# Performance work log

Measured on AMD Instinct MI355X. Metric: run time of the kernel, lower is better.

## Reference

```python
import jax, jax.numpy as jnp
import numpy as np

B, S, D, H = 4, 2048, 1024, 16
DK = D // H
THETA = 10000.0


def setup_inputs() -> dict:
    key = jax.random.key(0)
    ks = jax.random.split(key, 5)
    std = (2.0 / (D + D)) ** 0.5  # Linear init std (distribution differs from trunc-normal; math identical)
    x = jax.random.normal(ks[0], (B, S, D), dtype=jnp.float32)
    wq = jax.random.normal(ks[1], (D, D), dtype=jnp.float32) * std
    wk = jax.random.normal(ks[2], (D, D), dtype=jnp.float32) * std
    wv = jax.random.normal(ks[3], (D, D), dtype=jnp.float32) * std
    wo = jax.random.normal(ks[4], (D, D), dtype=jnp.float32) * std
    mask = jnp.tril(jnp.ones((S, S), dtype=bool))  # causal
    return {"x": x, "mask": mask, "wq": wq, "wk": wk, "wv": wv, "wo": wo}


def _rope(t):
    # t: [b, h, s, dk]; interleaved pairs (even, odd)
    s = t.shape[-2]
    inv_freq = THETA ** (-jnp.arange(0, DK, 2, dtype=jnp.float32) / DK)  # [dk/2]
    ang = jnp.arange(s, dtype=jnp.float32)[:, None] * inv_freq[None, :]  # [s, dk/2]
    cos = jnp.cos(ang)[None, None, :, :]
    sin = jnp.sin(ang)[None, None, :, :]
    x1 = t[..., 0::2]
    x2 = t[..., 1::2]
    rot = jnp.stack([x1 * cos - x2 * sin, x1 * sin + x2 * cos], axis=-1)
    return rot.reshape(t.shape)


def reference(x, mask, wq, wk, wv, wo):
    b, s, d = x.shape
    def heads(w):
        return jnp.einsum('bsd,ed->bse', x, w).reshape(b, s, H, DK).transpose(0, 2, 1, 3)
    q = _rope(heads(wq))
    k = _rope(heads(wk))
    v = heads(wv)
    scores = jnp.einsum('bhqd,bhkd->bhqk', q, k) / (DK ** 0.5)
    scores = jnp.where(mask, scores, -jnp.inf)
    attn = jax.nn.softmax(scores, axis=-1)
    out = jnp.einsum('bhqk,bhkd->bhqd', attn, v)
    out = out.transpose(0, 2, 1, 3).reshape(b, s, d)
    return jnp.einsum('bsd,ed->bse', out, wo)
```

## Files before the change

kernel.cpp:

```cpp
#include <hip/hip_runtime.h>

constexpr int Bc = 4, Sc = 2048, Dc = 1024, Hc = 16, DKc = 64;
constexpr int Mc = Bc * Sc;

typedef __bf16 bf16x8 __attribute__((ext_vector_type(8)));
typedef float f32x4 __attribute__((ext_vector_type(4)));
typedef unsigned short ush;

#define DEVI __device__ __forceinline__

DEVI ush bf(float f) { return __builtin_bit_cast(ush, (__bf16)f); }

DEVI void ld_lds16(const void* g, void* l) {
    __builtin_amdgcn_global_load_lds(
        (const __attribute__((address_space(1))) unsigned int*)g,
        (__attribute__((address_space(3))) unsigned int*)l,
        16, 0, 0);
}

constexpr unsigned CVT_BLOCKS = 6144;
constexpr unsigned TAB_BLOCKS = 32;

__global__ __launch_bounds__(256) void cvt_all(
    const float* __restrict__ x,  const float* __restrict__ wq,
    const float* __restrict__ wk, const float* __restrict__ wv,
    const float* __restrict__ wo, ush* __restrict__ dst,
    float2* __restrict__ csn)
{
    if (blockIdx.x >= CVT_BLOCKS) {
        int t = (int)(blockIdx.x - CVT_BLOCKS) * 256 + threadIdx.x;
#pragma unroll
        for (int i = 0; i < 8; i++) {
            int idx = t * 8 + i;
            int s = idx >> 5, p = idx & 31;
            float ang = (float)s * exp2f(-(float)p * 0.4152410118609203f);
            csn[idx] = make_float2(cosf(ang), sinf(ang));
        }
        return;
    }
    size_t t = ((size_t)blockIdx.x * 256 + threadIdx.x) * 8;
    const float* src; size_t loc;
    const size_t NX = (size_t)Mc * Dc;
    if (t < NX) { src = x; loc = t; }
    else {
        size_t u = t - NX;
        int wi = (int)(u >> 20);
        src = (wi == 0) ? wq : ((wi == 1) ? wk : ((wi == 2) ? wv : wo));
        loc = u & 1048575u;
    }
    float4 a = *(const float4*)(src + loc);
    float4 b = *(const float4*)(src + loc + 4);
    union { ush u[8]; float4 v; } o;
    o.u[0] = bf(a.x); o.u[1] = bf(a.y); o.u[2] = bf(a.z); o.u[3] = bf(a.w);
    o.u[4] = bf(b.x); o.u[5] = bf(b.y); o.u[6] = bf(b.z); o.u[7] = bf(b.w);
    *(float4*)(dst + t) = o.v;
}

template<int MODE>
__global__ __launch_bounds__(512, 4) void gemm_bf(
    const ush* __restrict__ A,
    const ush* __restrict__ W0, const ush* __restrict__ W1,
    const ush* __restrict__ W2,
    ush* __restrict__ Oq, ush* __restrict__ Ok, ush* __restrict__ Ovt,
    float* __restrict__ Of, const float2* __restrict__ csn)
{
    __shared__ ush sA[128 * 64];
    __shared__ ush sB[128 * 64];

    const int xcd = (int)blockIdx.x;
    const int u = (int)blockIdx.y + 64 * (int)blockIdx.z;
    const int z = (MODE == 0) ? (u >> 6) : 0;
    const int w = u & 63;
    const int m0 = (xcd * 8 + (w >> 3)) * 128;
    const int n0 = (w & 7) * 128;

    const ush* W = (z == 0) ? W0 : ((z == 1) ? W1 : W2);

    const int tid = threadIdx.x;
    const int wv = tid >> 6;
    const int ln = tid & 63;
    const int lr = ln & 15;
    const int lq = ln >> 4;
    const int wm = (wv & 1) * 64;
    const int wn = (wv >> 1) * 32;
    const int rL = ln >> 3;
    const int cSw = ((ln & 7) ^ rL) * 8;
    const int ca0 = lq ^ (ln & 7);

    f32x4 acc[4][2] = {};
    const bool swp = (MODE == 0) && (z == 2);

    for (int kt = 0; kt < 1024; kt += 64) {
        __syncthreads();
#pragma unroll
        for (int i = 0; i < 2; i++) {
            int chunk = wv * 2 + i;
            int rr = chunk * 8 + rL;
            ld_lds16(&A[(size_t)(m0 + rr) * 1024 + kt + cSw], &sA[chunk * 512]);
            ld_lds16(&W[(size_t)(n0 + rr) * 1024 + kt + cSw], &sB[chunk * 512]);
        }
        __syncthreads();
#pragma unroll
        for (int ks = 0; ks < 2; ks++) {
            const int cf = (ca0 ^ (ks << 2)) << 3;
            bf16x8 af[4], bfr[2];
#pragma unroll
            for (int t = 0; t < 4; t++)
                af[t]  = *(const bf16x8*)(&sA[(wm + t * 16 + lr) * 64 + cf]);
#pragma unroll
            for (int t = 0; t < 2; t++)
                bfr[t] = *(const bf16x8*)(&sB[(wn + t * 16 + lr) * 64 + cf]);
            __builtin_amdgcn_s_setprio(1);
            if (!swp) {
#pragma unroll
                for (int ia = 0; ia < 4; ia++)
#pragma unroll
                    for (int ib = 0; ib < 2; ib++)
                        acc[ia][ib] = __builtin_amdgcn_mfma_f32_16x16x32_bf16(
                            af[ia], bfr[ib], acc[ia][ib], 0, 0, 0);
            } else {
#pragma unroll
                for (int ia = 0; ia < 4; ia++)
#pragma unroll
                    for (int ib = 0; ib < 2; ib++)
                        acc[ia][ib] = __builtin_amdgcn_mfma_f32_16x16x32_bf16(
                            bfr[ib], af[ia], acc[ia][ib], 0, 0, 0);
            }
            __builtin_amdgcn_s_setprio(0);
        }
    }

    ush* Oqk = (z == 0) ? Oq : Ok;
#pragma unroll
    for (int ia = 0; ia < 4; ia++) {
#pragma unroll
        for (int ib = 0; ib < 2; ib++) {
#pragma unroll
            for (int r = 0; r < 4; r++) {
                float v = acc[ia][ib][r];
                if (MODE == 1) {
                    int m = m0 + wm + ia * 16 + lq * 4 + r;
                    int n = n0 + wn + ib * 16 + lr;
                    Of[(size_t)m * 1024 + n] = v;
                } else if (swp) {
                    int n = n0 + wn + ib * 16 + lq * 4 + r;
                    int m = m0 + wm + ia * 16 + lr;
                    Ovt[((size_t)((m >> 11) * Hc + (n >> 6)) * DKc + (n & 63)) * Sc
                        + (m & (Sc - 1))] = bf(v);
                } else {
                    int m = m0 + wm + ia * 16 + lq * 4 + r;
                    int n = n0 + wn + ib * 16 + lr;
                    float part = __shfl_xor(v, 1);
                    int dk = n & 63, s = m & (Sc - 1);
                    float2 cs = csn[(s << 5) + (dk >> 1)];
                    float res = (dk & 1) ? (part * cs.y + v * cs.x)
                                         : (v * cs.x - part * cs.y);
                    if (z == 0) res *= 0.18033688011112042f;
                    Oqk[((size_t)((m >> 11) * Hc + (n >> 6)) * Sc + s) * DKc + dk] = bf(res);
                }
            }
        }
    }
}

__global__ __launch_bounds__(512, 4) void attn_k(
    const ush* __restrict__ Q, const ush* __restrict__ Kr,
    const ush* __restrict__ Vt, ush* __restrict__ O)
{
    __shared__ ush kbuf[64 * 64];
    __shared__ ush vbuf[64 * 64];
    __shared__ ush pbuf[8][16 * 76];

    const int head = (int)blockIdx.x * 8 + ((int)blockIdx.y >> 3);
    const int qp   = (int)blockIdx.y & 7;
    const int tid = threadIdx.x;
    const int wv = tid >> 6;
    const int ln = tid & 63;
    const int lr = ln & 15;
    const int lq = ln >> 4;
    const size_t hoff = (size_t)head * Sc * DKc;
    const int rS = tid >> 3;
    const int c8 = tid & 7;
    const int cS = c8 * 8;
    const int cW = ((c8 ^ (rS & 7)) * 8);
    const int cw0 = ((lq ^ (lr & 7)) * 8);

#define LOADKV(ktv, kk, vv) {                                                \
        int kb_ = (ktv) * 64;                                                \
        kk = *(const float4*)(&Kr[hoff + (size_t)(kb_ + rS) * DKc + cS]);    \
        vv = *(const float4*)(&Vt[hoff + (size_t)rS * Sc + kb_ + cS]); }

#define WRITEKV(kk, vv) {                                                    \
        *(float4*)(&kbuf[rS * 64 + cW]) = kk;                                \
        *(float4*)(&vbuf[rS * 64 + cW]) = vv; }

#define COMPUTE(ktv) {                                                       \
        const int kb = (ktv) * 64;                                           \
        f32x4 sc[4];                                                         \
        __builtin_amdgcn_s_setprio(1);                                       \
        _Pragma("unroll")                                                    \
        for (int nt = 0; nt < 4; nt++) {                                     \
            const ush* kr_ = &kbuf[(nt * 16 + lr) * 64];                     \
            bf16x8 bk0 = *(const bf16x8*)(kr_ + cw0);                        \
            bf16x8 bk1 = *(const bf16x8*)(kr_ + (cw0 ^ 32));                 \
            f32x4 cc = {};                                                   \
            cc = __builtin_amdgcn_mfma_f32_16x16x32_bf16(aq0, bk0, cc, 0, 0, 0); \
            cc = __builtin_amdgcn_mfma_f32_16x16x32_bf16(aq1, bk1, cc, 0, 0, 0); \
            sc[nt] = cc;                                                     \
        }                                                                    \
        __builtin_amdgcn_s_setprio(0);                                       \
        const int rowq = qbase + wv * 16 + lq * 4;                           \
        const bool needmask = (kb + 63 > qbase + wv * 16);                   \
        _Pragma("unroll")                                                    \
        for (int nt = 0; nt < 4; nt++) {                                     \
            int col = kb + nt * 16 + lr;                                     \
            _Pragma("unroll")                                                \
            for (int r = 0; r < 4; r++) {                                    \
                float v = sc[nt][r];                                         \
                if (needmask && col > rowq + r) v = -1e30f;                  \
                float p = exp2f(v);                                          \
                sc[nt][r] = p;                                               \
                rs[r] += p;                                                  \
            }                                                                \
        }                                                                    \
        {                                                                    \
            ush* pb = pbuf[wv];                                              \
            _Pragma("unroll")                                                \
            for (int nt = 0; nt < 4; nt++)                                   \
                _Pragma("unroll")                                            \
                for (int r = 0; r < 4; r++)                                  \
                    pb[(lq * 4 + r) * 76 + nt * 16 + lr] = bf(sc[nt][r]);    \
            __builtin_amdgcn_s_setprio(1);                                   \
            _Pragma("unroll")                                                \
            for (int ks = 0; ks < 2; ks++) {                                 \
                bf16x8 ap = *(const bf16x8*)(&pb[lr * 76 + ks * 32 + lq * 8]); \
                _Pragma("unroll")                                            \
                for (int nt = 0; nt < 4; nt++) {                             \
                    bf16x8 bv = *(const bf16x8*)(&vbuf[(nt * 16 + lr) * 64   \
                                                       + (cw0 ^ (ks * 32))]); \
                    oacc[nt] = __builtin_amdgcn_mfma_f32_16x16x32_bf16(      \
                        ap, bv, oacc[nt], 0, 0, 0);                          \
                }                                                            \
            }                                                                \
            __builtin_amdgcn_s_setprio(0);                                   \
        }                                                                    \
    }

    for (int half = 0; half < 2; half++) {
        const int qt = half ? (15 - qp) : qp;
        const int qbase = qt * 128;
        const int kmax = 2 * qt + 2;

        bf16x8 aq0, aq1;
        {
            int row = qbase + wv * 16 + lr;
            const ush* qp_ = &Q[hoff + (size_t)row * DKc + lq * 8];
            aq0 = *(const bf16x8*)(qp_);
            aq1 = *(const bf16x8*)(qp_ + 32);
        }

        f32x4 oacc[4] = {};
        float rs[4] = {};

        float4 ka, va, kb2, vb2;

        LOADKV(0, ka, va);
        int kt = 0;
        while (true) {
            __syncthreads();
            WRITEKV(ka, va);
            __syncthreads();
            if (kt + 1 < kmax) LOADKV(kt + 1, kb2, vb2);
            COMPUTE(kt);
            kt++;
            if (kt >= kmax) break;
            __syncthreads();
            WRITEKV(kb2, vb2);
            __syncthreads();
            if (kt + 1 < kmax) LOADKV(kt + 1, ka, va);
            COMPUTE(kt);
            kt++;
            if (kt >= kmax) break;
        }

        const int b = head >> 4, h = head & 15;
#pragma unroll
        for (int r = 0; r < 4; r++) {
            float l = rs[r];
#pragma unroll
            for (int d = 1; d < 16; d <<= 1) l += __shfl_xor(l, d);
            float inv = 1.0f / l;
            int srow = qbase + wv * 16 + lq * 4 + r;
#pragma unroll
            for (int nt = 0; nt < 4; nt++) {
                int e = h * 64 + nt * 16 + lr;
                O[((size_t)(b * Sc + srow)) * Dc + e] = bf(oacc[nt][r] * inv);
            }
        }
    }
#undef LOADKV
#undef WRITEKV
#undef COMPUTE
}

extern "C" void kernel_launch(void* const* d_in, const int* in_sizes, int n_in,
                              void* d_out, int out_size, void* d_ws, size_t ws_size,
                              hipStream_t stream)
{
    (void)in_sizes; (void)n_in; (void)out_size; (void)ws_size;
    const float* x  = (const float*)d_in[0];
    const float* wq = (const float*)d_in[2];
    const float* wk = (const float*)d_in[3];
    const float* wv = (const float*)d_in[4];
    const float* wo = (const float*)d_in[5];

    const size_t N = (size_t)Mc * Dc;
    const size_t NW = (size_t)Dc * Dc;

    ush* xh  = (ush*)d_ws;
    ush* wqh = xh  + N;
    ush* wkh = wqh + NW;
    ush* wvh = wkh + NW;
    ush* woh = wvh + NW;
    ush* vt  = woh + NW;
    ush* ows = vt  + N;
    float2* csn = (float2*)(ows + N);
    ush* qd = (ush*)d_out;
    ush* kd = qd + N;

    cvt_all<<<dim3(CVT_BLOCKS + TAB_BLOCKS), 256, 0, stream>>>(
        x, wq, wk, wv, wo, xh, csn);
    gemm_bf<0><<<dim3(8, 64, 3), 512, 0, stream>>>(
        xh, wqh, wkh, wvh, qd, kd, vt, nullptr, csn);
    attn_k<<<dim3(8, 64), 512, 0, stream>>>(qd, kd, vt, ows);
    gemm_bf<1><<<dim3(8, 64, 1), 512, 0, stream>>>(
        ows, woh, woh, woh, nullptr, nullptr, nullptr, (float*)d_out, csn);
}
```

Before: 291.1 us.

## Double-buffer K/V tiles in LDS with one barrier per tile

The attention kernel's K and V shared-memory tiles are now double-buffered. The next tile is written into the alternate buffer while the current one is being computed, which replaces two __syncthreads per key tile with a single barrier that waits only on LDS traffic. The aim is to cut synchronisation stalls and let LDS writes overlap with MFMA work. In exchange, LDS use per block roughly doubles for K/V, which may limit occupancy, and the global loads now run two tiles ahead in registers.

```diff
diff --git a/kernel.cpp b/kernel.cpp
--- a/kernel.cpp
+++ b/kernel.cpp
@@ -167,8 +167,8 @@
     const ush* __restrict__ Q, const ush* __restrict__ Kr,
     const ush* __restrict__ Vt, ush* __restrict__ O)
 {
-    __shared__ ush kbuf[64 * 64];
-    __shared__ ush vbuf[64 * 64];
+    __shared__ ush kbuf[2][64 * 64];
+    __shared__ ush vbuf[2][64 * 64];
     __shared__ ush pbuf[8][16 * 76];
 
     const int head = (int)blockIdx.x * 8 + ((int)blockIdx.y >> 3);
@@ -185,22 +185,26 @@
     const int cW = ((c8 ^ (rS & 7)) * 8);
     const int cw0 = ((lq ^ (lr & 7)) * 8);
 
+#define BARRIER() { asm volatile("s_waitcnt lgkmcnt(0)" ::: "memory");       \
+        __builtin_amdgcn_sched_barrier(0);                                   \
+        __builtin_amdgcn_s_barrier(); }
+
 #define LOADKV(ktv, kk, vv) {                                                \
         int kb_ = (ktv) * 64;                                                \
         kk = *(const float4*)(&Kr[hoff + (size_t)(kb_ + rS) * DKc + cS]);    \
         vv = *(const float4*)(&Vt[hoff + (size_t)rS * Sc + kb_ + cS]); }
 
-#define WRITEKV(kk, vv) {                                                    \
-        *(float4*)(&kbuf[rS * 64 + cW]) = kk;                                \
-        *(float4*)(&vbuf[rS * 64 + cW]) = vv; }
-
-#define COMPUTE(ktv) {                                                       \
+#define WRITEKV(bb, kk, vv) {                                                \
+        *(float4*)(&kbuf[bb][rS * 64 + cW]) = kk;                            \
+        *(float4*)(&vbuf[bb][rS * 64 + cW]) = vv; }
+
+#define COMPUTE(bb, ktv) {                                                   \
         const int kb = (ktv) * 64;                                           \
         f32x4 sc[4];                                                         \
         __builtin_amdgcn_s_setprio(1);                                       \
         _Pragma("unroll")                                                    \
         for (int nt = 0; nt < 4; nt++) {                                     \
-            const ush* kr_ = &kbuf[(nt * 16 + lr) * 64];                     \
+            const ush* kr_ = &kbuf[bb][(nt * 16 + lr) * 64];                 \
             bf16x8 bk0 = *(const bf16x8*)(kr_ + cw0);                        \
             bf16x8 bk1 = *(const bf16x8*)(kr_ + (cw0 ^ 32));                 \
             f32x4 cc = {};                                                   \
@@ -236,7 +240,7 @@
                 bf16x8 ap = *(const bf16x8*)(&pb[lr * 76 + ks * 32 + lq * 8]); \
                 _Pragma("unroll")                                            \
                 for (int nt = 0; nt < 4; nt++) {                             \
-                    bf16x8 bv = *(const bf16x8*)(&vbuf[(nt * 16 + lr) * 64   \
+                    bf16x8 bv = *(const bf16x8*)(&vbuf[bb][(nt * 16 + lr) * 64 \
                                                        + (cw0 ^ (ks * 32))]); \
                     oacc[nt] = __builtin_amdgcn_mfma_f32_16x16x32_bf16(      \
                         ap, bv, oacc[nt], 0, 0, 0);                          \
@@ -265,20 +269,22 @@
         float4 ka, va, kb2, vb2;
 
         LOADKV(0, ka, va);
+        WRITEKV(0, ka, va);
+        if (kmax > 1) LOADKV(1, kb2, vb2);
+        BARRIER();
+
         int kt = 0;
         while (true) {
-            __syncthreads();
-            WRITEKV(ka, va);
-            __syncthreads();
-            if (kt + 1 < kmax) LOADKV(kt + 1, kb2, vb2);
-            COMPUTE(kt);
+            if (kt + 1 < kmax) WRITEKV(1, kb2, vb2);
+            if (kt + 2 < kmax) LOADKV(kt + 2, ka, va);
+            COMPUTE(0, kt);
+            BARRIER();
             kt++;
             if (kt >= kmax) break;
-            __syncthreads();
-            WRITEKV(kb2, vb2);
-            __syncthreads();
-            if (kt + 1 < kmax) LOADKV(kt + 1, ka, va);
-            COMPUTE(kt);
+            if (kt + 1 < kmax) WRITEKV(0, ka, va);
+            if (kt + 2 < kmax) LOADKV(kt + 2, kb2, vb2);
+            COMPUTE(1, kt);
+            BARRIER();
             kt++;
             if (kt >= kmax) break;
         }
@@ -298,6 +304,7 @@
             }
         }
     }
+#undef BARRIER
 #undef LOADKV
 #undef WRITEKV
 #undef COMPUTE
```

Measured after the change: 292.9 us. Within noise of the previous version (+0.6%).
